# Optimization experiments

Hardware: AMD Instinct MI355X
Metric: run time of the kernel (lower is better)

## Reference

```python
import jax, jax.numpy as jnp
from jax import lax
import numpy as np

D_COND = 48      # d_condition
K = 24           # n_bins
HID = 128        # hidden_dim
T = 10           # n_transforms
TAIL = 15.0      # tail_bound
B = 131072       # batch (contexts x samples flattened, as in sample())


def setup_inputs() -> dict:
    key = jax.random.key(0)
    ks = jax.random.split(key, 8)
    def w(k, shape, fan_in, gain=1.0):
        return (jax.random.normal(k, shape, jnp.float32) * (gain / np.sqrt(fan_in))).astype(jnp.float32)
    return {
        "z": jax.random.normal(ks[0], (B,), jnp.float32),
        "context": jax.random.normal(ks[1], (B, D_COND), jnp.float32),
        "W0": w(ks[2], (T, D_COND, HID), D_COND),
        "b0": jnp.zeros((T, HID), jnp.float32),
        "W1": w(ks[3], (T, HID, HID), HID),
        "b1": jnp.zeros((T, HID), jnp.float32),
        "W2": w(ks[4], (T, HID, HID), HID),
        "b2": jnp.zeros((T, HID), jnp.float32),
        "W3": w(ks[5], (T, HID, 3 * K + 1), HID, gain=0.1),
        "b3": jnp.zeros((T, 3 * K + 1), jnp.float32),
        "loc": jnp.float32(85.0),
        "scale": jnp.float32(5.0),
    }


def _spline_forward(x, widths, heights, derivs):
    # x: (B,); widths/heights: (B,K); derivs: (B,K+1)
    inside = (x >= -TAIL) & (x <= TAIL)
    cw = jnp.pad(jnp.cumsum(widths, -1), ((0, 0), (1, 0)), constant_values=-TAIL)   # (B,K+1)
    ch = jnp.pad(jnp.cumsum(heights, -1), ((0, 0), (1, 0)), constant_values=-TAIL)  # (B,K+1)
    # torch.searchsorted(cw[...,1:], x, right=False) == count of elems < x
    idx = jnp.clip(jnp.sum(cw[:, 1:] < x[:, None], axis=-1), 0, K - 1)
    take = lambda a, i: jnp.take_along_axis(a, i[:, None], axis=-1)[:, 0]
    w_k = take(widths, idx)
    h_k = take(heights, idx)
    cw_k = take(cw, idx)
    ch_k = take(ch, idx)
    d_k = take(derivs, idx)
    d_k1 = take(derivs, idx + 1)
    s = h_k / w_k
    xi = jnp.clip((x - cw_k) / w_k, 1e-6, 1.0 - 1e-6)
    one_m = 1.0 - xi
    numer = h_k * (s * xi * xi + d_k * xi * one_m)
    denom = s + (d_k + d_k1 - 2.0 * s) * xi * one_m
    y = ch_k + numer / denom
    dy_dxi = s * s * (d_k1 * xi * xi + 2.0 * s * xi * one_m + d_k * one_m * one_m) / (denom * denom)
    log_det = (jnp.log(jnp.maximum(dy_dxi, 1e-10))
               + jnp.log(jnp.maximum(h_k, 1e-10))
               - jnp.log(jnp.maximum(w_k, 1e-10)))
    y = jnp.where(inside, y, x)
    log_det = jnp.where(inside, log_det, 0.0)
    return y, log_det


def reference(z, context, W0, b0, W1, b1, W2, b2, W3, b3, loc, scale):
    def body(carry, p):
        zc, ld = carry
        w0, c0, w1, c1, w2, c2, w3, c3 = p
        h = jax.nn.silu(context @ w0 + c0)
        h = jax.nn.silu(h @ w1 + c1)
        h = jax.nn.silu(h @ w2 + c2)
        params = h @ w3 + c3                                   # (B, 3K+1)
        Wl, Hl, Dl = params[:, :K], params[:, K:2 * K], params[:, 2 * K:]
        widths = jax.nn.softmax(Wl, axis=-1) * (2.0 * TAIL)
        heights = jax.nn.softmax(Hl, axis=-1) * (2.0 * TAIL)
        derivs = jax.nn.softplus(Dl) + 1e-3
        y, l = _spline_forward(zc, widths, heights, derivs)
        return (y, ld + l), None

    (z_out, total_ld), _ = lax.scan(body, (z, jnp.zeros_like(z)),
                                    (W0, b0, W1, b1, W2, b2, W3, b3))
    s = jnp.maximum(scale, 0.1)
    temp_f = z_out * s + loc   # _unstandardize, as in sample()
    return temp_f, total_ld
```

## Files before the change

### kernel.cpp

```cpp
#include <hip/hip_runtime.h>
#include <hip/hip_bf16.h>

#define DCOND 48
#define KBINS 24
#define HID 128
#define TSTEPS 10
#define NPAR 73
#define TAILF 15.0f

typedef __attribute__((ext_vector_type(8))) short v8s;
typedef __attribute__((ext_vector_type(4))) float f32x4;

__device__ __forceinline__ short f2bf(float f) {
    __hip_bfloat16 h = __float2bfloat16(f);
    return __builtin_bit_cast(short, h);
}
__device__ __forceinline__ float bf2f(short s) {
    unsigned u = ((unsigned)(unsigned short)s) << 16;
    return __builtin_bit_cast(float, u);
}
__device__ __forceinline__ float silu_f(float v) {
    return __fdividef(v, 1.0f + __expf(-v));
}

__global__ void prep_w(const float* __restrict__ W0, const float* __restrict__ W1,
                       const float* __restrict__ W2, const float* __restrict__ W3,
                       short* __restrict__ ws)
{
    int g = blockIdx.x * 256 + threadIdx.x;
    if (g >= TSTEPS * 51200) return;
    int t = g / 51200;
    int r = g % 51200;

    int base_e, elems, NT, Kreal, Nreal;
    const float* W;
    if (r < 8192)       { base_e = 0;     elems = 8192;  NT = 8; Kreal = 48;  Nreal = 128; W = W0 + (size_t)t * DCOND * HID; }
    else if (r < 24576) { base_e = 8192;  elems = 16384; NT = 8; Kreal = 128; Nreal = 128; W = W1 + (size_t)t * HID * HID; }
    else if (r < 40960) { base_e = 24576; elems = 16384; NT = 8; Kreal = 128; Nreal = 128; W = W2 + (size_t)t * HID * HID; }
    else                { base_e = 40960; elems = 10240; NT = 5; Kreal = 128; Nreal = 73;  W = W3 + (size_t)t * HID * NPAR; }

    int e  = r - base_e;
    int j  = e & 7;
    int ln = (e >> 3) & 63;
    int q  = e >> 9;
    int nt = q % NT, kc = q / NT;
    int k  = kc * 32 + (ln >> 4) * 8 + j;
    int n  = nt * 16 + (ln & 15);

    float v = 0.0f;
    if (k < Kreal && n < Nreal) v = W[(size_t)k * Nreal + n];
    short hi = f2bf(v);
    short lo = f2bf(v - bf2f(hi));

    size_t o = (size_t)t * 102400 + 2 * (size_t)base_e + e;
    ws[o]         = hi;
    ws[o + elems] = lo;
}

#define MBLK 128
#define NTHR 512

__device__ __forceinline__ void w_write_chunk(short* dst, const short* src) {
    *(v8s*)dst = *(const v8s*)src;
}

template<int ROUNDS>
__device__ __forceinline__ void w_issue(const short* __restrict__ g, int tid, v8s (&r)[8]) {
    #pragma unroll
    for (int i = 0; i < ROUNDS; ++i)
        r[i] = *(const v8s*)(g + tid * 8 + i * 4096);
}
template<int ROUNDS>
__device__ __forceinline__ void w_flush(short* __restrict__ lds, int tid, const v8s (&r)[8]) {
    #pragma unroll
    for (int i = 0; i < ROUNDS; ++i)
        *(v8s*)(lds + tid * 8 + i * 4096) = r[i];
}

template<int KC, int NT, bool ACT>
__device__ __forceinline__ void layer_run(const float* __restrict__ bias, int nreal,
                                          float* __restrict__ Hlds,
                                          const short* __restrict__ Wlds,
                                          int lane, int wave)
{
    constexpr int ELEMS = KC * NT * 512;
    const int arow = wave * 16 + (lane & 15);
    const int asw  = (arow & 7) << 4;
    const int kgrp = (lane >> 4) * 8;

    v8s ah[KC], al[KC];
    #pragma unroll
    for (int kc = 0; kc < KC; ++kc) {
        const int kb4 = (kc * 32 + kgrp) * 4;
        f32x4 a0 = *(const f32x4*)((const char*)Hlds + arow * 512 + (kb4 ^ asw));
        f32x4 a1 = *(const f32x4*)((const char*)Hlds + arow * 512 + ((kb4 + 16) ^ asw));
        #pragma unroll
        for (int u = 0; u < 4; ++u) {
            short h0 = f2bf(a0[u]); ah[kc][u]     = h0; al[kc][u]     = f2bf(a0[u] - bf2f(h0));
            short h1 = f2bf(a1[u]); ah[kc][4 + u] = h1; al[kc][4 + u] = f2bf(a1[u] - bf2f(h1));
        }
    }

    const int crow0 = wave * 16 + (lane >> 4) * 4;
    const int ncol  = lane & 15;

    #pragma unroll
    for (int np = 0; np < NT / 2; ++np) {
        const int nt0 = np * 2, nt1 = np * 2 + 1;
        const int n0 = nt0 * 16 + ncol, n1 = nt1 * 16 + ncol;
        const float bv0 = (n0 < nreal) ? bias[n0] : 0.0f;
        const float bv1 = (n1 < nreal) ? bias[n1] : 0.0f;
        f32x4 acc0 = {bv0, bv0, bv0, bv0};
        f32x4 acc1 = {bv1, bv1, bv1, bv1};
        #pragma unroll
        for (int kc = 0; kc < KC; ++kc) {
            const short* bp0 = Wlds + ((size_t)(kc * NT + nt0) * 64 + lane) * 8;
            const short* bp1 = Wlds + ((size_t)(kc * NT + nt1) * 64 + lane) * 8;
            v8s bh0 = *(const v8s*)bp0;
            v8s bl0 = *(const v8s*)(bp0 + ELEMS);
            v8s bh1 = *(const v8s*)bp1;
            v8s bl1 = *(const v8s*)(bp1 + ELEMS);
            acc0 = __builtin_amdgcn_mfma_f32_16x16x32_bf16(ah[kc], bh0, acc0, 0, 0, 0);
            acc1 = __builtin_amdgcn_mfma_f32_16x16x32_bf16(ah[kc], bh1, acc1, 0, 0, 0);
            acc0 = __builtin_amdgcn_mfma_f32_16x16x32_bf16(ah[kc], bl0, acc0, 0, 0, 0);
            acc1 = __builtin_amdgcn_mfma_f32_16x16x32_bf16(ah[kc], bl1, acc1, 0, 0, 0);
            acc0 = __builtin_amdgcn_mfma_f32_16x16x32_bf16(al[kc], bh0, acc0, 0, 0, 0);
            acc1 = __builtin_amdgcn_mfma_f32_16x16x32_bf16(al[kc], bh1, acc1, 0, 0, 0);
        }
        #pragma unroll
        for (int r = 0; r < 4; ++r) {
            const int row = crow0 + r;
            const int sw  = (row & 7) << 4;
            float v0 = acc0[r], v1 = acc1[r];
            if (ACT) { v0 = silu_f(v0); v1 = silu_f(v1); }
            *(float*)((char*)Hlds + row * 512 + ((n0 * 4) ^ sw)) = v0;
            *(float*)((char*)Hlds + row * 512 + ((n1 * 4) ^ sw)) = v1;
        }
    }
    if (NT & 1) {
        const int nt = NT - 1;
        const int n0 = nt * 16 + ncol;
        const float bv0 = (n0 < nreal) ? bias[n0] : 0.0f;
        f32x4 acc0 = {bv0, bv0, bv0, bv0};
        #pragma unroll
        for (int kc = 0; kc < KC; ++kc) {
            const short* bp0 = Wlds + ((size_t)(kc * NT + nt) * 64 + lane) * 8;
            v8s bh0 = *(const v8s*)bp0;
            v8s bl0 = *(const v8s*)(bp0 + ELEMS);
            acc0 = __builtin_amdgcn_mfma_f32_16x16x32_bf16(ah[kc], bh0, acc0, 0, 0, 0);
            acc0 = __builtin_amdgcn_mfma_f32_16x16x32_bf16(ah[kc], bl0, acc0, 0, 0, 0);
            acc0 = __builtin_amdgcn_mfma_f32_16x16x32_bf16(al[kc], bh0, acc0, 0, 0, 0);
        }
        #pragma unroll
        for (int r = 0; r < 4; ++r) {
            const int row = crow0 + r;
            const int sw  = (row & 7) << 4;
            float v0 = acc0[r];
            if (ACT) v0 = silu_f(v0);
            *(float*)((char*)Hlds + row * 512 + ((n0 * 4) ^ sw)) = v0;
        }
    }
}

__global__ __launch_bounds__(NTHR, 1)
void nsf_mfma(const float* __restrict__ z_g, const float* __restrict__ ctx_g,
              const float* __restrict__ b0g, const float* __restrict__ b1g,
              const float* __restrict__ b2g, const float* __restrict__ b3g,
              const float* __restrict__ locp, const float* __restrict__ sclp,
              const short* __restrict__ wsW, float* __restrict__ out, int B)
{
    __shared__ float Hlds[MBLK * 128];
    __shared__ short Wlds[32768];
    const int tid  = threadIdx.x;
    const int lane = tid & 63, wave = tid >> 6;
    const int blk  = blockIdx.x;

    float x = 0.0f, ld = 0.0f;
    if (tid < MBLK) {
        int gid = blk * MBLK + tid;
        if (gid > B - 1) gid = B - 1;
        x = z_g[gid];
    }

    v8s wreg[8];

    #pragma unroll 1
    for (int t = 0; t < TSTEPS; ++t) {
        const short* wstep = wsW + (size_t)t * 102400;

        w_issue<4>(wstep, tid, wreg);

        {
            const int row = tid >> 2, q = tid & 3;
            int gs = blk * MBLK + row;
            if (gs > B - 1) gs = B - 1;
            const float* cg = ctx_g + (size_t)gs * DCOND + q * 12;
            f32x4 c0 = *(const f32x4*)cg;
            f32x4 c1 = *(const f32x4*)(cg + 4);
            f32x4 c2 = *(const f32x4*)(cg + 8);
            const int sw = (row & 7) << 4;
            char* hb = (char*)Hlds + row * 512;
            *(f32x4*)(hb + ((q * 48)      ^ sw)) = c0;
            *(f32x4*)(hb + ((q * 48 + 16) ^ sw)) = c1;
            *(f32x4*)(hb + ((q * 48 + 32) ^ sw)) = c2;
            f32x4 zz = {0, 0, 0, 0};
            *(f32x4*)(hb + ((192 + q * 16) ^ sw)) = zz;
        }

        w_flush<4>(Wlds, tid, wreg);
        w_issue<8>(wstep + 16384, tid, wreg);
        __syncthreads();

        layer_run<2, 8, true>(b0g + t * HID, HID, Hlds, Wlds, lane, wave);
        __syncthreads();

        w_flush<8>(Wlds, tid, wreg);
        w_issue<8>(wstep + 49152, tid, wreg);
        __syncthreads();

        layer_run<4, 8, true>(b1g + t * HID, HID, Hlds, Wlds, lane, wave);
        __syncthreads();

        w_flush<8>(Wlds, tid, wreg);
        w_issue<5>(wstep + 81920, tid, wreg);
        __syncthreads();

        layer_run<4, 8, true>(b2g + t * HID, HID, Hlds, Wlds, lane, wave);
        __syncthreads();

        w_flush<5>(Wlds, tid, wreg);
        __syncthreads();

        layer_run<4, 5, false>(b3g + t * NPAR, NPAR, Hlds, Wlds, lane, wave);
        __syncthreads();

        if (tid < MBLK) {
            const char* hrow = (const char*)Hlds + tid * 512;
            const int sw = (tid & 7) << 4;

            float pw[KBINS];
            #pragma unroll
            for (int i = 0; i < KBINS; ++i) pw[i] = *(const float*)(hrow + ((i * 4) ^ sw));
            float mw = pw[0];
            #pragma unroll
            for (int i = 1; i < KBINS; ++i) mw = fmaxf(mw, pw[i]);
            float wsum = 0.0f;
            #pragma unroll
            for (int i = 0; i < KBINS; ++i) { pw[i] = __expf(pw[i] - mw); wsum += pw[i]; }
            const float wmul = __fdividef(2.0f * TAILF, wsum);

            float ph[KBINS];
            #pragma unroll
            for (int i = 0; i < KBINS; ++i) ph[i] = *(const float*)(hrow + (((KBINS + i) * 4) ^ sw));
            float mh = ph[0];
            #pragma unroll
            for (int i = 1; i < KBINS; ++i) mh = fmaxf(mh, ph[i]);
            float hsum = 0.0f;
            #pragma unroll
            for (int i = 0; i < KBINS; ++i) { ph[i] = __expf(ph[i] - mh); hsum += ph[i]; }
            const float hmul = __fdividef(2.0f * TAILF, hsum);

            float dv[KBINS + 1];
            #pragma unroll
            for (int i = 0; i <= KBINS; ++i) {
                float xd = *(const float*)(hrow + (((2 * KBINS + i) * 4) ^ sw));
                dv[i] = fmaxf(xd, 0.0f) + __logf(1.0f + __expf(-fabsf(xd))) + 0.001f;
            }

            float cw = 0.0f, ch = 0.0f;
            float cwk = -TAILF, chk = -TAILF;
            float wk = pw[0] * wmul, hk = ph[0] * hmul, dk = dv[0], dk1 = dv[1];
            #pragma unroll
            for (int i = 1; i < KBINS; ++i) {
                cw += pw[i - 1] * wmul;
                ch += ph[i - 1] * hmul;
                if (cw < x) {
                    cwk = cw; chk = ch;
                    wk = pw[i] * wmul; hk = ph[i] * hmul;
                    dk = dv[i]; dk1 = dv[i + 1];
                }
            }

            const bool inside = (x >= -TAILF) && (x <= TAILF);
            const float sr = __fdividef(hk, wk);
            float xi = __fdividef(x - cwk, wk);
            xi = fminf(fmaxf(xi, 1e-6f), 1.0f - 1e-6f);
            const float om  = 1.0f - xi;
            const float xio = xi * om;
            const float numer = hk * (sr * xi * xi + dk * xio);
            const float denom = sr + (dk + dk1 - 2.0f * sr) * xio;
            const float y = chk + __fdividef(numer, denom);
            const float dyd = __fdividef(sr * sr * (dk1 * xi * xi + 2.0f * sr * xio + dk * om * om),
                                         denom * denom);
            const float lg = __logf(fmaxf(dyd, 1e-10f)) + __logf(fmaxf(hk, 1e-10f))
                           - __logf(fmaxf(wk, 1e-10f));
            x  = inside ? y : x;
            ld += inside ? lg : 0.0f;
        }
        __syncthreads();
    }

    if (tid < MBLK) {
        const int gid = blk * MBLK + tid;
        if (gid < B) {
            const float s = fmaxf(sclp[0], 0.1f);
            out[gid]     = fmaf(x, s, locp[0]);
            out[B + gid] = ld;
        }
    }
}

#define FBLK 256
template<int KIN, int WS, int NOUT, bool ACT>
__device__ __forceinline__ void dense_chunk(const float* __restrict__ W,
                                            const float* __restrict__ bias,
                                            int j0, const float (&hin)[KIN],
                                            float* __restrict__ sb, int tid)
{
    #pragma unroll 1
    for (int jj = 0; jj < NOUT; jj += 8) {
        const int j = j0 + jj;
        float a[8];
        #pragma unroll
        for (int u = 0; u < 8; ++u) a[u] = bias[j + u];
        #pragma unroll
        for (int k = 0; k < KIN; ++k) {
            const float* w = W + k * WS + j;
            const float hk = hin[k];
            #pragma unroll
            for (int u = 0; u < 8; ++u) a[u] = fmaf(hk, w[u], a[u]);
        }
        #pragma unroll
        for (int u = 0; u < 8; ++u) {
            float v = ACT ? silu_f(a[u]) : a[u];
            sb[(jj + u) * FBLK + tid] = v;
        }
    }
}

__global__ __launch_bounds__(FBLK, 2)
void nsf_fwd_slow(const float* __restrict__ z_g, const float* __restrict__ ctx_g,
                  const float* __restrict__ W0g, const float* __restrict__ b0g,
                  const float* __restrict__ W1g, const float* __restrict__ b1g,
                  const float* __restrict__ W2g, const float* __restrict__ b2g,
                  const float* __restrict__ W3g, const float* __restrict__ b3g,
                  const float* __restrict__ locp, const float* __restrict__ sclp,
                  float* __restrict__ out, int B)
{
    __shared__ float sbuf[64 * FBLK];
    const int tid = threadIdx.x;
    const int gid = blockIdx.x * FBLK + tid;
    if (gid >= B) return;
    float x = z_g[gid], ld = 0.0f;
    #pragma unroll 1
    for (int t = 0; t < TSTEPS; ++t) {
        asm volatile("" ::: "memory");
        const float* W0 = W0g + (size_t)t * DCOND * HID;
        const float* b0 = b0g + (size_t)t * HID;
        const float* W1 = W1g + (size_t)t * HID * HID;
        const float* b1 = b1g + (size_t)t * HID;
        const float* W2 = W2g + (size_t)t * HID * HID;
        const float* b2 = b2g + (size_t)t * HID;
        const float* W3 = W3g + (size_t)t * HID * NPAR;
        const float* b3 = b3g + (size_t)t * NPAR;
        float ctx[DCOND];
        #pragma unroll
        for (int k = 0; k < DCOND; ++k) ctx[k] = ctx_g[(size_t)gid * DCOND + k];
        float h[HID];
        dense_chunk<DCOND, HID, 64, true>(W0, b0, 0, ctx, sbuf, tid);
        #pragma unroll
        for (int j = 0; j < 64; ++j) h[j] = sbuf[j * FBLK + tid];
        dense_chunk<DCOND, HID, 64, true>(W0, b0, 64, ctx, sbuf, tid);
        #pragma unroll
        for (int j = 0; j < 64; ++j) h[64 + j] = sbuf[j * FBLK + tid];
        #pragma unroll 1
        for (int l = 0; l < 2; ++l) {
            const float* W  = (l == 0) ? W1 : W2;
            const float* bb = (l == 0) ? b1 : b2;
            float hlo[64];
            dense_chunk<HID, HID, 64, true>(W, bb, 0, h, sbuf, tid);
            #pragma unroll
            for (int j = 0; j < 64; ++j) hlo[j] = sbuf[j * FBLK + tid];
            dense_chunk<HID, HID, 64, true>(W, bb, 64, h, sbuf, tid);
            #pragma unroll
            for (int j = 0; j < 64; ++j) h[64 + j] = sbuf[j * FBLK + tid];
            #pragma unroll
            for (int j = 0; j < 64; ++j) h[j] = hlo[j];
        }
        float p[NPAR];
        dense_chunk<HID, NPAR, 64, false>(W3, b3, 0, h, sbuf, tid);
        #pragma unroll
        for (int j = 0; j < 64; ++j) p[j] = sbuf[j * FBLK + tid];
        dense_chunk<HID, NPAR, 8, false>(W3, b3, 64, h, sbuf, tid);
        #pragma unroll
        for (int j = 0; j < 8; ++j) p[64 + j] = sbuf[j * FBLK + tid];
        {
            float a = b3[72];
            #pragma unroll
            for (int k = 0; k < HID; ++k) a = fmaf(h[k], W3[k * NPAR + 72], a);
            p[72] = a;
        }
        float mw = p[0];
        #pragma unroll
        for (int i = 1; i < KBINS; ++i) mw = fmaxf(mw, p[i]);
        float we[KBINS]; float wsum = 0.0f;
        #pragma unroll
        for (int i = 0; i < KBINS; ++i) { we[i] = __expf(p[i] - mw); wsum += we[i]; }
        const float wmul = __fdividef(2.0f * TAILF, wsum);
        float mh = p[KBINS];
        #pragma unroll
        for (int i = 1; i < KBINS; ++i) mh = fmaxf(mh, p[KBINS + i]);
        float he[KBINS]; float hsum = 0.0f;
        #pragma unroll
        for (int i = 0; i < KBINS; ++i) { he[i] = __expf(p[KBINS + i] - mh); hsum += he[i]; }
        const float hmul = __fdividef(2.0f * TAILF, hsum);
        float dvv[KBINS + 1];
        #pragma unroll
        for (int i = 0; i <= KBINS; ++i) {
            float xd = p[2 * KBINS + i];
            dvv[i] = fmaxf(xd, 0.0f) + __logf(1.0f + __expf(-fabsf(xd))) + 0.001f;
        }
        float cw = 0.0f, ch = 0.0f, cwk = -TAILF, chk = -TAILF;
        float wk = we[0] * wmul, hk = he[0] * hmul, dk = dvv[0], dk1 = dvv[1];
        #pragma unroll
        for (int i = 1; i < KBINS; ++i) {
            cw += we[i - 1] * wmul;
            ch += he[i - 1] * hmul;
            if (cw < x) {
                cwk = cw; chk = ch;
                wk = we[i] * wmul; hk = he[i] * hmul;
                dk = dvv[i]; dk1 = dvv[i + 1];
            }
        }
        const bool inside = (x >= -TAILF) && (x <= TAILF);
        const float sr = __fdividef(hk, wk);
        float xi = __fdividef(x - cwk, wk);
        xi = fminf(fmaxf(xi, 1e-6f), 1.0f - 1e-6f);
        const float om  = 1.0f - xi;
        const float xio = xi * om;
        const float numer = hk * (sr * xi * xi + dk * xio);
        const float denom = sr + (dk + dk1 - 2.0f * sr) * xio;
        const float y = chk + __fdividef(numer, denom);
        const float dyd = __fdividef(sr * sr * (dk1 * xi * xi + 2.0f * sr * xio + dk * om * om),
                                     denom * denom);
        const float lg = __logf(fmaxf(dyd, 1e-10f)) + __logf(fmaxf(hk, 1e-10f))
                       - __logf(fmaxf(wk, 1e-10f));
        x  = inside ? y : x;
        ld += inside ? lg : 0.0f;
    }
    const float s = fmaxf(sclp[0], 0.1f);
    out[gid]     = fmaf(x, s, locp[0]);
    out[B + gid] = ld;
}

extern "C" void kernel_launch(void* const* d_in, const int* in_sizes, int n_in,
                              void* d_out, int out_size, void* d_ws, size_t ws_size,
                              hipStream_t stream) {
    const float* z    = (const float*)d_in[0];
    const float* ctx  = (const float*)d_in[1];
    const float* W0   = (const float*)d_in[2];
    const float* b0   = (const float*)d_in[3];
    const float* W1   = (const float*)d_in[4];
    const float* b1   = (const float*)d_in[5];
    const float* W2   = (const float*)d_in[6];
    const float* b2   = (const float*)d_in[7];
    const float* W3   = (const float*)d_in[8];
    const float* b3   = (const float*)d_in[9];
    const float* loc  = (const float*)d_in[10];
    const float* scl  = (const float*)d_in[11];
    float* out = (float*)d_out;
    const int B = in_sizes[0];

    const size_t ws_need = (size_t)TSTEPS * 102400 * sizeof(short);
    if (ws_size < ws_need) {
        const int nblk = (B + FBLK - 1) / FBLK;
        hipLaunchKernelGGL(nsf_fwd_slow, dim3(nblk), dim3(FBLK), 0, stream,
                           z, ctx, W0, b0, W1, b1, W2, b2, W3, b3, loc, scl, out, B);
        return;
    }

    short* ws = (short*)d_ws;
    const int prep_total = TSTEPS * 51200;
    hipLaunchKernelGGL(prep_w, dim3((prep_total + 255) / 256), dim3(256), 0, stream,
                       W0, W1, W2, W3, ws);

    const int nblk = (B + MBLK - 1) / MBLK;
    hipLaunchKernelGGL(nsf_mfma, dim3(nblk), dim3(NTHR), 0, stream,
                       z, ctx, b0, b1, b2, b3, loc, scl, ws, out, B);
}
```

Before: 642.7 us.

## Keep context fragments in registers, prefetch next step weights, spread spline across waves

The context is loaded once, split into bf16 hi/lo fragments held in registers for layer 0, so it is no longer reloaded and written to LDS every step. The next step's first weight chunk is prefetched during the final layer. The spline epilogue now runs on 16 lanes of every wave, reading its own rows without a block barrier, and applies softplus only to the two selected derivatives. Packed bf16 conversion instructions replace scalar conversions, and launch bounds now allow two blocks per CU, which may raise register pressure.

```diff
diff --git a/kernel.cpp b/kernel.cpp
--- a/kernel.cpp
+++ b/kernel.cpp
@@ -10,6 +10,7 @@
 
 typedef __attribute__((ext_vector_type(8))) short v8s;
 typedef __attribute__((ext_vector_type(4))) float f32x4;
+typedef __attribute__((ext_vector_type(4))) unsigned u32x4;
 
 __device__ __forceinline__ short f2bf(float f) {
     __hip_bfloat16 h = __float2bfloat16(f);
@@ -21,6 +22,33 @@
 }
 __device__ __forceinline__ float silu_f(float v) {
     return __fdividef(v, 1.0f + __expf(-v));
+}
+
+__device__ __forceinline__ unsigned cvt_pk(float a, float b) {
+    unsigned r;
+    asm("v_cvt_pk_bf16_f32 %0, %1, %2" : "=v"(r) : "v"(a), "v"(b));
+    return r;
+}
+
+__device__ __forceinline__ void split8(f32x4 a0, f32x4 a1, v8s& hi, v8s& lo) {
+    unsigned h0 = cvt_pk(a0[0], a0[1]);
+    unsigned h1 = cvt_pk(a0[2], a0[3]);
+    unsigned h2 = cvt_pk(a1[0], a1[1]);
+    unsigned h3 = cvt_pk(a1[2], a1[3]);
+    float l0 = a0[0] - __builtin_bit_cast(float, h0 << 16);
+    float l1 = a0[1] - __builtin_bit_cast(float, h0 & 0xffff0000u);
+    float l2 = a0[2] - __builtin_bit_cast(float, h1 << 16);
+    float l3 = a0[3] - __builtin_bit_cast(float, h1 & 0xffff0000u);
+    float l4 = a1[0] - __builtin_bit_cast(float, h2 << 16);
+    float l5 = a1[1] - __builtin_bit_cast(float, h2 & 0xffff0000u);
+    float l6 = a1[2] - __builtin_bit_cast(float, h3 << 16);
+    float l7 = a1[3] - __builtin_bit_cast(float, h3 & 0xffff0000u);
+    unsigned q0 = cvt_pk(l0, l1);
+    unsigned q1 = cvt_pk(l2, l3);
+    unsigned q2 = cvt_pk(l4, l5);
+    unsigned q3 = cvt_pk(l6, l7);
+    hi = __builtin_bit_cast(v8s, (u32x4){h0, h1, h2, h3});
+    lo = __builtin_bit_cast(v8s, (u32x4){q0, q1, q2, q3});
 }
 
 __global__ void prep_w(const float* __restrict__ W0, const float* __restrict__ W1,
@@ -60,10 +88,6 @@
 #define MBLK 128
 #define NTHR 512
 
-__device__ __forceinline__ void w_write_chunk(short* dst, const short* src) {
-    *(v8s*)dst = *(const v8s*)src;
-}
-
 template<int ROUNDS>
 __device__ __forceinline__ void w_issue(const short* __restrict__ g, int tid, v8s (&r)[8]) {
     #pragma unroll
@@ -77,27 +101,28 @@
         *(v8s*)(lds + tid * 8 + i * 4096) = r[i];
 }
 
-template<int KC, int NT, bool ACT>
+template<int KC, int NT, int ELEMS, bool ACT, bool AREG>
 __device__ __forceinline__ void layer_run(const float* __restrict__ bias, int nreal,
                                           float* __restrict__ Hlds,
-                                          const short* __restrict__ Wlds,
-                                          int lane, int wave)
+                                          const short* __restrict__ Wb,
+                                          int lane, int wave,
+                                          const v8s* cxh, const v8s* cxl)
 {
-    constexpr int ELEMS = KC * NT * 512;
     const int arow = wave * 16 + (lane & 15);
     const int asw  = (arow & 7) << 4;
-    const int kgrp = (lane >> 4) * 8;
+    const int kg   = (lane >> 4) * 8;
 
     v8s ah[KC], al[KC];
-    #pragma unroll
-    for (int kc = 0; kc < KC; ++kc) {
-        const int kb4 = (kc * 32 + kgrp) * 4;
-        f32x4 a0 = *(const f32x4*)((const char*)Hlds + arow * 512 + (kb4 ^ asw));
-        f32x4 a1 = *(const f32x4*)((const char*)Hlds + arow * 512 + ((kb4 + 16) ^ asw));
-        #pragma unroll
-        for (int u = 0; u < 4; ++u) {
-            short h0 = f2bf(a0[u]); ah[kc][u]     = h0; al[kc][u]     = f2bf(a0[u] - bf2f(h0));
-            short h1 = f2bf(a1[u]); ah[kc][4 + u] = h1; al[kc][4 + u] = f2bf(a1[u] - bf2f(h1));
+    if (AREG) {
+        #pragma unroll
+        for (int kc = 0; kc < KC; ++kc) { ah[kc] = cxh[kc]; al[kc] = cxl[kc]; }
+    } else {
+        #pragma unroll
+        for (int kc = 0; kc < KC; ++kc) {
+            const int kb = (kc * 32 + kg) * 4;
+            f32x4 a0 = *(const f32x4*)((const char*)Hlds + arow * 512 + (kb ^ asw));
+            f32x4 a1 = *(const f32x4*)((const char*)Hlds + arow * 512 + ((kb + 16) ^ asw));
+            split8(a0, a1, ah[kc], al[kc]);
         }
     }
 
@@ -114,8 +139,8 @@
         f32x4 acc1 = {bv1, bv1, bv1, bv1};
         #pragma unroll
         for (int kc = 0; kc < KC; ++kc) {
-            const short* bp0 = Wlds + ((size_t)(kc * NT + nt0) * 64 + lane) * 8;
-            const short* bp1 = Wlds + ((size_t)(kc * NT + nt1) * 64 + lane) * 8;
+            const short* bp0 = Wb + ((size_t)(kc * NT + nt0) * 64 + lane) * 8;
+            const short* bp1 = Wb + ((size_t)(kc * NT + nt1) * 64 + lane) * 8;
             v8s bh0 = *(const v8s*)bp0;
             v8s bl0 = *(const v8s*)(bp0 + ELEMS);
             v8s bh1 = *(const v8s*)bp1;
@@ -144,7 +169,7 @@
         f32x4 acc0 = {bv0, bv0, bv0, bv0};
         #pragma unroll
         for (int kc = 0; kc < KC; ++kc) {
-            const short* bp0 = Wlds + ((size_t)(kc * NT + nt) * 64 + lane) * 8;
+            const short* bp0 = Wb + ((size_t)(kc * NT + nt) * 64 + lane) * 8;
             v8s bh0 = *(const v8s*)bp0;
             v8s bl0 = *(const v8s*)(bp0 + ELEMS);
             acc0 = __builtin_amdgcn_mfma_f32_16x16x32_bf16(ah[kc], bh0, acc0, 0, 0, 0);
@@ -162,7 +187,7 @@
     }
 }
 
-__global__ __launch_bounds__(NTHR, 1)
+__global__ __launch_bounds__(NTHR, 2)
 void nsf_mfma(const float* __restrict__ z_g, const float* __restrict__ ctx_g,
               const float* __restrict__ b0g, const float* __restrict__ b1g,
               const float* __restrict__ b2g, const float* __restrict__ b3g,
@@ -175,101 +200,101 @@
     const int lane = tid & 63, wave = tid >> 6;
     const int blk  = blockIdx.x;
 
+    v8s wreg[8];
+    w_issue<4>(wsW, tid, wreg);
+
+    v8s cxh[2], cxl[2];
+    {
+        const int arow = wave * 16 + (lane & 15);
+        int gidr = blk * MBLK + arow;
+        if (gidr > B - 1) gidr = B - 1;
+        const int k0 = (lane >> 4) * 8;
+        const float* cg = ctx_g + (size_t)gidr * DCOND;
+        f32x4 c0 = *(const f32x4*)(cg + k0);
+        f32x4 c1 = *(const f32x4*)(cg + k0 + 4);
+        split8(c0, c1, cxh[0], cxl[0]);
+        if ((lane >> 4) < 2) {
+            f32x4 c2 = *(const f32x4*)(cg + 32 + k0);
+            f32x4 c3 = *(const f32x4*)(cg + 36 + k0);
+            split8(c2, c3, cxh[1], cxl[1]);
+        } else {
+            #pragma unroll
+            for (int u = 0; u < 8; ++u) { cxh[1][u] = 0; cxl[1][u] = 0; }
+        }
+    }
+
     float x = 0.0f, ld = 0.0f;
-    if (tid < MBLK) {
-        int gid = blk * MBLK + tid;
+    if (lane < 16) {
+        int gid = blk * MBLK + wave * 16 + lane;
         if (gid > B - 1) gid = B - 1;
         x = z_g[gid];
     }
-
-    v8s wreg[8];
 
     #pragma unroll 1
     for (int t = 0; t < TSTEPS; ++t) {
         const short* wstep = wsW + (size_t)t * 102400;
-
-        w_issue<4>(wstep, tid, wreg);
-
-        {
-            const int row = tid >> 2, q = tid & 3;
-            int gs = blk * MBLK + row;
-            if (gs > B - 1) gs = B - 1;
-            const float* cg = ctx_g + (size_t)gs * DCOND + q * 12;
-            f32x4 c0 = *(const f32x4*)cg;
-            f32x4 c1 = *(const f32x4*)(cg + 4);
-            f32x4 c2 = *(const f32x4*)(cg + 8);
-            const int sw = (row & 7) << 4;
-            char* hb = (char*)Hlds + row * 512;
-            *(f32x4*)(hb + ((q * 48)      ^ sw)) = c0;
-            *(f32x4*)(hb + ((q * 48 + 16) ^ sw)) = c1;
-            *(f32x4*)(hb + ((q * 48 + 32) ^ sw)) = c2;
-            f32x4 zz = {0, 0, 0, 0};
-            *(f32x4*)(hb + ((192 + q * 16) ^ sw)) = zz;
-        }
+        const short* wnext = wsW + (size_t)((t + 1) % TSTEPS) * 102400;
 
         w_flush<4>(Wlds, tid, wreg);
         w_issue<8>(wstep + 16384, tid, wreg);
         __syncthreads();
 
-        layer_run<2, 8, true>(b0g + t * HID, HID, Hlds, Wlds, lane, wave);
+        layer_run<2, 8, 8192, true, true>(b0g + t * HID, HID, Hlds, Wlds,
+                                          lane, wave, cxh, cxl);
         __syncthreads();
 
         w_flush<8>(Wlds, tid, wreg);
         w_issue<8>(wstep + 49152, tid, wreg);
         __syncthreads();
 
-        layer_run<4, 8, true>(b1g + t * HID, HID, Hlds, Wlds, lane, wave);
+        layer_run<4, 8, 16384, true, false>(b1g + t * HID, HID, Hlds, Wlds,
+                                            lane, wave, nullptr, nullptr);
         __syncthreads();
 
         w_flush<8>(Wlds, tid, wreg);
         w_issue<5>(wstep + 81920, tid, wreg);
         __syncthreads();
 
-        layer_run<4, 8, true>(b2g + t * HID, HID, Hlds, Wlds, lane, wave);
+        layer_run<4, 8, 16384, true, false>(b2g + t * HID, HID, Hlds, Wlds,
+                                            lane, wave, nullptr, nullptr);
         __syncthreads();
 
         w_flush<5>(Wlds, tid, wreg);
-        __syncthreads();
-
-        layer_run<4, 5, false>(b3g + t * NPAR, NPAR, Hlds, Wlds, lane, wave);
-        __syncthreads();
-
-        if (tid < MBLK) {
-            const char* hrow = (const char*)Hlds + tid * 512;
-            const int sw = (tid & 7) << 4;
-
-            float pw[KBINS];
-            #pragma unroll
-            for (int i = 0; i < KBINS; ++i) pw[i] = *(const float*)(hrow + ((i * 4) ^ sw));
-            float mw = pw[0];
-            #pragma unroll
-            for (int i = 1; i < KBINS; ++i) mw = fmaxf(mw, pw[i]);
-            float wsum = 0.0f;
-            #pragma unroll
-            for (int i = 0; i < KBINS; ++i) { pw[i] = __expf(pw[i] - mw); wsum += pw[i]; }
+        w_issue<4>(wnext, tid, wreg);
+        __syncthreads();
+
+        layer_run<4, 5, 10240, false, false>(b3g + t * NPAR, NPAR, Hlds, Wlds,
+                                             lane, wave, nullptr, nullptr);
+
+        if (lane < 16) {
+            const int rowS = wave * 16 + lane;
+            const char* hrow = (const char*)Hlds + rowS * 512;
+            const int sw = (rowS & 7) << 4;
+
+            float pw[KBINS], ph[KBINS];
+            #pragma unroll
+            for (int g = 0; g < 6; ++g) {
+                f32x4 vw = *(const f32x4*)(hrow + ((g * 16) ^ sw));
+                f32x4 vh = *(const f32x4*)(hrow + (((g + 6) * 16) ^ sw));
+                #pragma unroll
+                for (int u = 0; u < 4; ++u) { pw[g * 4 + u] = vw[u]; ph[g * 4 + u] = vh[u]; }
+            }
+            float mw = pw[0], mh = ph[0];
+            #pragma unroll
+            for (int i = 1; i < KBINS; ++i) { mw = fmaxf(mw, pw[i]); mh = fmaxf(mh, ph[i]); }
+            float wsum = 0.0f, hsum = 0.0f;
+            #pragma unroll
+            for (int i = 0; i < KBINS; ++i) {
+                pw[i] = __expf(pw[i] - mw); wsum += pw[i];
+                ph[i] = __expf(ph[i] - mh); hsum += ph[i];
+            }
             const float wmul = __fdividef(2.0f * TAILF, wsum);
-
-            float ph[KBINS];
-            #pragma unroll
-            for (int i = 0; i < KBINS; ++i) ph[i] = *(const float*)(hrow + (((KBINS + i) * 4) ^ sw));
-            float mh = ph[0];
-            #pragma unroll
-            for (int i = 1; i < KBINS; ++i) mh = fmaxf(mh, ph[i]);
-            float hsum = 0.0f;
-            #pragma unroll
-            for (int i = 0; i < KBINS; ++i) { ph[i] = __expf(ph[i] - mh); hsum += ph[i]; }
             const float hmul = __fdividef(2.0f * TAILF, hsum);
-
-            float dv[KBINS + 1];
-            #pragma unroll
-            for (int i = 0; i <= KBINS; ++i) {
-                float xd = *(const float*)(hrow + (((2 * KBINS + i) * 4) ^ sw));
-                dv[i] = fmaxf(xd, 0.0f) + __logf(1.0f + __expf(-fabsf(xd))) + 0.001f;
-            }
 
             float cw = 0.0f, ch = 0.0f;
             float cwk = -TAILF, chk = -TAILF;
-            float wk = pw[0] * wmul, hk = ph[0] * hmul, dk = dv[0], dk1 = dv[1];
+            float wk = pw[0] * wmul, hk = ph[0] * hmul;
+            int idx = 0;
             #pragma unroll
             for (int i = 1; i < KBINS; ++i) {
                 cw += pw[i - 1] * wmul;
@@ -277,9 +302,13 @@
                 if (cw < x) {
                     cwk = cw; chk = ch;
                     wk = pw[i] * wmul; hk = ph[i] * hmul;
-                    dk = dv[i]; dk1 = dv[i + 1];
+                    idx = i;
                 }
             }
+            float d0 = *(const float*)(hrow + (((2 * KBINS + idx) * 4) ^ sw));
+            float d1 = *(const float*)(hrow + (((2 * KBINS + idx + 1) * 4) ^ sw));
+            const float dk  = fmaxf(d0, 0.0f) + __logf(1.0f + __expf(-fabsf(d0))) + 0.001f;
+            const float dk1 = fmaxf(d1, 0.0f) + __logf(1.0f + __expf(-fabsf(d1))) + 0.001f;
 
             const bool inside = (x >= -TAILF) && (x <= TAILF);
             const float sr = __fdividef(hk, wk);
@@ -300,8 +329,8 @@
         __syncthreads();
     }
 
-    if (tid < MBLK) {
-        const int gid = blk * MBLK + tid;
+    if (lane < 16) {
+        const int gid = blk * MBLK + wave * 16 + lane;
         if (gid < B) {
             const float s = fmaxf(sclp[0], 0.1f);
             out[gid]     = fmaf(x, s, locp[0]);
```

Result: faster. 627.7 us (-2.3%).
